# Performance work log

Hardware: AMD Instinct MI355X
Metric: run time of the kernel (lower is better)

The kernel has to match this reference:

```python
import jax, jax.numpy as jnp
import numpy as np

N_NODES = 50000
N_EDGES = 800000
D = 128


def gin_layer(x, edge_index, edge_attr, ee1, ee2, W1, b1, W2, b2):
    # PyG default flow source_to_target: x_j = x[edge_index[0]], aggregate at edge_index[1]
    src, dst = edge_index[0], edge_index[1]
    edge_emb = ee1[edge_attr[:, 0]] + ee2[edge_attr[:, 1]]           # [E, D]
    msg = x[src] + edge_emb                                          # [E, D]
    aggr = jax.ops.segment_sum(msg, dst, num_segments=x.shape[0])    # [N, D]
    h = jax.nn.relu(aggr @ W1 + b1)                                  # [N, 2D]
    return h @ W2 + b2                                               # [N, out]


def setup_inputs() -> dict:
    key = jax.random.key(0)
    ks = jax.random.split(key, 16)
    s = 1.0 / np.sqrt(D)
    inp = {
        "x": jax.random.normal(ks[0], (N_NODES, D), jnp.float32),
        "edge_index": jax.random.randint(ks[1], (2, N_EDGES), 0, N_NODES, dtype=jnp.int32),
        "edge_attr": jax.random.randint(ks[2], (N_EDGES, 2), 0, 3, dtype=jnp.int32),
        "ee1_0": jax.random.normal(ks[3], (6, D), jnp.float32) * s,
        "ee2_0": jax.random.normal(ks[4], (3, D), jnp.float32) * s,
        "W1_0": jax.random.normal(ks[5], (D, 2 * D), jnp.float32) * s,
        "b1_0": jnp.zeros((2 * D,), jnp.float32),
        "W2_0": jax.random.normal(ks[6], (2 * D, D), jnp.float32) * s,
        "b2_0": jnp.zeros((D,), jnp.float32),
        "ee1_1": jax.random.normal(ks[7], (6, D), jnp.float32) * s,
        "ee2_1": jax.random.normal(ks[8], (3, D), jnp.float32) * s,
        "W1_1": jax.random.normal(ks[9], (D, 2 * D), jnp.float32) * s,
        "b1_1": jnp.zeros((2 * D,), jnp.float32),
        "W2_1": jax.random.normal(ks[10], (2 * D, D), jnp.float32) * s,
        "b2_1": jnp.zeros((D,), jnp.float32),
    }
    return inp


def reference(x, edge_index, edge_attr, ee1_0, ee2_0, W1_0, b1_0, W2_0, b2_0,
              ee1_1, ee2_1, W1_1, b1_1, W2_1, b2_1):
    h = gin_layer(x, edge_index, edge_attr, ee1_0, ee2_0, W1_0, b1_0, W2_0, b2_0)
    h = jax.nn.relu(h)  # activation between GNN layers
    out = gin_layer(h, edge_index, edge_attr, ee1_1, ee2_1, W1_1, b1_1, W2_1, b2_1)
    return out  # jk='last'
```

## Files before the change

kernel.cpp:

```cpp
#include <hip/hip_runtime.h>

typedef __attribute__((ext_vector_type(8))) short s16x8;
typedef __attribute__((ext_vector_type(4))) float f32x4;
typedef unsigned short u16;
typedef unsigned char u8;
typedef unsigned long long u64;

#define D_FEAT 128
#define TILE1 4096

__device__ __forceinline__ u16 f2bf(float f) {
    unsigned u = __builtin_bit_cast(unsigned, f);
    u = u + 0x7fffu + ((u >> 16) & 1u);
    return (u16)(u >> 16);
}

__global__ __launch_bounds__(256) void prep_kernel(
        const float4* __restrict__ X4, u16* __restrict__ xb, int n4, int nbA,
        const int* __restrict__ dst, int* __restrict__ ghist, int E, int nb1, int bins,
        const float* __restrict__ ee1_0, const float* __restrict__ ee2_0,
        const float* __restrict__ ee1_1, const float* __restrict__ ee2_1,
        float* __restrict__ emb,
        const float* __restrict__ W1_0, const float* __restrict__ W2_0,
        const float* __restrict__ W1_1, const float* __restrict__ W2_1,
        u16* __restrict__ wout) {
    __shared__ int h[256];
    const int t = threadIdx.x;
    int b = blockIdx.x;

    if (b < nbA) {
        for (int i = b * 256 + t; i < n4; i += nbA * 256) {
            float4 v = X4[i];
            uint2 p;
            p.x = (unsigned)f2bf(v.x) | ((unsigned)f2bf(v.y) << 16);
            p.y = (unsigned)f2bf(v.z) | ((unsigned)f2bf(v.w) << 16);
            *(uint2*)(xb + (size_t)i * 4) = p;
        }
        return;
    }
    b -= nbA;
    if (b < nb1) {
        h[t] = 0;
        __syncthreads();
        const int base = b * TILE1;
        #pragma unroll
        for (int j = 0; j < TILE1 / 256; ++j) {
            int e = base + j * 256 + t;
            if (e < E) atomicAdd(&h[dst[e] >> 8], 1);
        }
        __syncthreads();
        if (t < bins) ghist[t * nb1 + b] = h[t];
        return;
    }
    b -= nb1;
    if (b < 18) {
        int gi = b * 256 + t;
        int layer = gi / 2304;
        int rem = gi - layer * 2304;
        int code = rem >> 7;
        int d = rem & 127;
        int a0 = code / 3, a1 = code - a0 * 3;
        const float* e1 = layer ? ee1_1 : ee1_0;
        const float* e2 = layer ? ee2_1 : ee2_0;
        emb[layer * 2304 + code * 128 + d] = e1[a0 * 128 + d] + e2[a1 * 128 + d];
        return;
    }
    b -= 18;
    {
        int mat = b >> 7;
        const float* s = (mat == 0) ? W1_0 : (mat == 1) ? W2_0 : (mat == 2) ? W1_1 : W2_1;
        int K = (mat & 1) ? 256 : 128;
        int Nc = 384 - K;
        u16* d = wout + mat * 32768;
        int idx = (b & 127) * 256 + t;
        int n = idx / K, k = idx - n * K;
        d[idx] = f2bf(s[k * Nc + n]);
    }
}

__global__ __launch_bounds__(256) void scan1a_kernel(int* __restrict__ ghist,
                                                     int* __restrict__ btot, int nb1) {
    __shared__ int wt[4];
    const int t = threadIdx.x, lane = t & 63, wid = t >> 6;
    const int bin = blockIdx.x;
    const int v = (t < nb1) ? ghist[bin * nb1 + t] : 0;
    int s = v;
    #pragma unroll
    for (int off = 1; off < 64; off <<= 1) {
        int u = __shfl_up(s, off, 64);
        if (lane >= off) s += u;
    }
    if (lane == 63) wt[wid] = s;
    __syncthreads();
    int add = 0;
    #pragma unroll
    for (int w = 0; w < 4; ++w) add += (w < wid) ? wt[w] : 0;
    s += add;
    if (t < nb1) ghist[bin * nb1 + t] = s - v;
    if (t == 255) btot[bin] = s;
}

__global__ __launch_bounds__(256) void scatter1_kernel(const int* __restrict__ src,
                                                       const int* __restrict__ dst,
                                                       const int* __restrict__ eattr,
                                                       const int* __restrict__ ghist,
                                                       const int* __restrict__ btot,
                                                       u64* __restrict__ buf1,
                                                       int E, int nb1, int bins) {
    __shared__ int lofs[256];
    __shared__ int wt[4];
    const int t = threadIdx.x, lane = t & 63, wid = t >> 6;
    const int v = (t < bins) ? btot[t] : 0;
    int s = v;
    #pragma unroll
    for (int off = 1; off < 64; off <<= 1) {
        int u = __shfl_up(s, off, 64);
        if (lane >= off) s += u;
    }
    if (lane == 63) wt[wid] = s;
    __syncthreads();
    int add = 0;
    #pragma unroll
    for (int w = 0; w < 4; ++w) add += (w < wid) ? wt[w] : 0;
    s += add;
    if (t < bins) lofs[t] = (s - v) + ghist[t * nb1 + blockIdx.x];
    __syncthreads();

    const int base = blockIdx.x * TILE1;
    #pragma unroll
    for (int j = 0; j < TILE1 / 256; ++j) {
        int e = base + j * 256 + t;
        if (e < E) {
            int d = dst[e];
            int2 at = ((const int2*)eattr)[e];
            unsigned pay = (unsigned)src[e] | ((unsigned)(at.x * 3 + at.y) << 16);
            int pos = atomicAdd(&lofs[d >> 8], 1);
            buf1[pos] = ((u64)(unsigned)d << 32) | pay;
        }
    }
}

__global__ __launch_bounds__(1024) void bucket2_kernel(const u64* __restrict__ buf1,
                                                       const int* __restrict__ btot,
                                                       int* __restrict__ row_start,
                                                       unsigned* __restrict__ edges,
                                                       unsigned* __restrict__ countsw,
                                                       int N, int bins) {
    __shared__ int cnt[256];
    __shared__ int cur[256];
    __shared__ int wts[4];
    __shared__ unsigned ccnt[256 * 18];
    __shared__ int sb[2];
    const int t = threadIdx.x, lane = t & 63, wid = t >> 6;
    const int bin = blockIdx.x;

    int v0 = 0, s0 = 0;
    if (t < 256) {
        v0 = (t < bins) ? btot[t] : 0;
        s0 = v0;
        #pragma unroll
        for (int off = 1; off < 64; off <<= 1) {
            int u = __shfl_up(s0, off, 64);
            if (lane >= off) s0 += u;
        }
        if (lane == 63) wts[wid] = s0;
        cnt[t] = 0;
    }
    for (int i = t; i < 256 * 18; i += 1024) ccnt[i] = 0;
    __syncthreads();
    if (t < 256) {
        int add = 0;
        #pragma unroll
        for (int w = 0; w < 4; ++w) add += (w < wid) ? wts[w] : 0;
        s0 += add;
        if (t == bin) { sb[0] = s0 - v0; sb[1] = s0; }
    }
    __syncthreads();
    const int lo = sb[0], hi = sb[1];

    for (int i = lo + t; i < hi; i += 1024)
        atomicAdd(&cnt[(int)(buf1[i] >> 32) & 255], 1);
    __syncthreads();

    int v1 = 0, s1 = 0;
    if (t < 256) {
        v1 = cnt[t];
        s1 = v1;
        #pragma unroll
        for (int off = 1; off < 64; off <<= 1) {
            int u = __shfl_up(s1, off, 64);
            if (lane >= off) s1 += u;
        }
        if (lane == 63) wts[wid] = s1;
    }
    __syncthreads();
    if (t < 256) {
        int add = 0;
        #pragma unroll
        for (int w = 0; w < 4; ++w) add += (w < wid) ? wts[w] : 0;
        s1 += add;
        const int g = bin * 256 + t;
        if (g < N) row_start[g + 1] = lo + s1;
        cur[t] = s1 - v1;
        if (bin == 0 && t == 0) row_start[0] = 0;
    }
    __syncthreads();

    for (int i = lo + t; i < hi; i += 1024) {
        u64 rec = buf1[i];
        const int local = (int)(rec >> 32) & 255;
        int loc = atomicAdd(&cur[local], 1);
        edges[lo + loc] = (unsigned)rec;
        atomicAdd(&ccnt[local * 18 + ((unsigned)rec >> 16)], 1);
    }
    __syncthreads();

    if (t < 256) {
        const int g = bin * 256 + t;
        if (g < N) {
            unsigned w[5] = {0, 0, 0, 0, 0};
            #pragma unroll
            for (int c = 0; c < 18; ++c)
                w[c >> 2] |= ccnt[t * 18 + c] << (8 * (c & 3));
            #pragma unroll
            for (int k = 0; k < 5; ++k)
                countsw[(size_t)g * 5 + k] = w[k];
        }
    }
}

__global__ __launch_bounds__(256) void aggregate_kernel(const u16* __restrict__ X,
                                                        const int* __restrict__ row_start,
                                                        const unsigned* __restrict__ edges,
                                                        const float* __restrict__ emb,
                                                        const unsigned* __restrict__ countsw,
                                                        u16* __restrict__ A, int N) {
    __shared__ float semb[18 * 128];
    for (int i = threadIdx.x; i < 18 * 128; i += 256) semb[i] = emb[i];
    __syncthreads();
    const int lane = threadIdx.x & 63;
    const int wstart = blockIdx.x * 4 + (threadIdx.x >> 6);
    const int wstride = gridDim.x * 4;
    const float2* sem2 = (const float2*)semb;

    for (int node = wstart; node < N; node += wstride) {
        unsigned cw[5];
        #pragma unroll
        for (int k = 0; k < 5; ++k) cw[k] = countsw[(size_t)node * 5 + k];

        int s = __builtin_amdgcn_readfirstlane(row_start[node]);
        const int e = __builtin_amdgcn_readfirstlane(row_start[node + 1]);
        float a0 = 0.f, a1 = 0.f;

        while (s < e) {
            const int take = (e - s < 64) ? (e - s) : 64;
            unsigned pl = edges[s + (lane < take ? lane : 0)];
            #pragma unroll
            for (int c = 0; c < 4; ++c) {
                const int cb = c * 16;
                if (cb < take) {
                    unsigned ps[16];
                    unsigned xv[16];
                    #pragma unroll
                    for (int j = 0; j < 16; ++j)
                        ps[j] = __builtin_amdgcn_readlane(pl, cb + j);
                    #pragma unroll
                    for (int j = 0; j < 16; ++j)
                        xv[j] = *(const unsigned*)(X + (ps[j] & 0xFFFFu) * D_FEAT + lane * 2);
                    #pragma unroll
                    for (int j = 0; j < 16; ++j) {
                        const float m = (cb + j < take) ? 1.f : 0.f;
                        a0 += m * __builtin_bit_cast(float, xv[j] << 16);
                        a1 += m * __builtin_bit_cast(float, xv[j] & 0xFFFF0000u);
                    }
                }
            }
            s += take;
        }

        #pragma unroll
        for (int w = 0; w < 5; ++w) {
            #pragma unroll
            for (int b = 0; b < 4; ++b) {
                const int code = w * 4 + b;
                if (code < 18) {
                    const float cf = (float)((cw[w] >> (8 * b)) & 255u);
                    float2 ev = sem2[code * 64 + lane];
                    a0 += cf * ev.x;
                    a1 += cf * ev.y;
                }
            }
        }

        unsigned outp = (unsigned)f2bf(a0) | ((unsigned)f2bf(a1) << 16);
        *(unsigned*)(A + (size_t)node * D_FEAT + lane * 2) = outp;
    }
}

template <bool RELU2, bool OUTF32>
__global__ __launch_bounds__(256, 1) void mlp_kernel(const u16* __restrict__ A,
                                                     const u16* __restrict__ B1t,
                                                     const float* __restrict__ bias1,
                                                     const u16* __restrict__ B2t,
                                                     const float* __restrict__ bias2,
                                                     void* __restrict__ C, int M, int nt) {
    extern __shared__ __align__(16) u16 lds[];
    u16* w1 = lds;
    u16* w2 = lds + 32768;
    u16* hh = lds + 65536;
    const int tid = threadIdx.x;
    const int wave = tid >> 6;
    const int lane = tid & 63;
    const int m16 = lane & 15;
    const int quad = lane >> 4;

    {
        const uint4* src1 = (const uint4*)B1t;
        const uint4* src2 = (const uint4*)B2t;
        #pragma unroll
        for (int i = 0; i < 16; ++i) {
            int s = i * 256 + tid;
            uint4 v = src1[s];
            int c = (((s >> 8) * 4 + ((s >> 2) & 3)) << 6) | ((s & 3) << 4) | ((s >> 4) & 15);
            *(uint4*)(w1 + c * 8) = v;
        }
        #pragma unroll
        for (int i = 0; i < 16; ++i) {
            int s = i * 256 + tid;
            uint4 v = src2[s];
            int c = (((s >> 9) * 8 + ((s >> 2) & 7)) << 6) | ((s & 3) << 4) | ((s >> 5) & 15);
            *(uint4*)(w2 + c * 8) = v;
        }
    }
    float b1v[16];
    #pragma unroll
    for (int t = 0; t < 16; ++t) b1v[t] = bias1[t * 16 + m16];
    float b2v[8];
    #pragma unroll
    for (int t = 0; t < 8; ++t) b2v[t] = bias2[t * 16 + m16];

    const int hbase = wave * 4096;

    int tile = blockIdx.x;
    s16x8 af[4];
    #pragma unroll
    for (int kb = 0; kb < 4; ++kb) af[kb] = s16x8{};
    if (tile < nt) {
        const int arow = tile * 64 + wave * 16 + m16;
        if (arow < M) {
            #pragma unroll
            for (int kb = 0; kb < 4; ++kb)
                af[kb] = *(const s16x8*)(A + (size_t)arow * 128 + kb * 32 + quad * 8);
        }
    }

    __syncthreads();

    for (; tile < nt; tile += 256) {
        const int row0 = tile * 64 + wave * 16;

        f32x4 acc[16];
        #pragma unroll
        for (int t = 0; t < 16; ++t) acc[t] = f32x4{0, 0, 0, 0};
        #pragma unroll
        for (int kb = 0; kb < 4; ++kb) {
            #pragma unroll
            for (int t = 0; t < 16; ++t) {
                s16x8 bf = *(const s16x8*)(w1 + (((((t << 2) | kb) << 6) | lane) * 8));
                acc[t] = __builtin_amdgcn_mfma_f32_16x16x32_bf16(af[kb], bf, acc[t], 0, 0, 0);
            }
        }

        const int ntile = tile + 256;
        s16x8 afn[4];
        #pragma unroll
        for (int kb = 0; kb < 4; ++kb) afn[kb] = s16x8{};
        if (ntile < nt) {
            const int arow = ntile * 64 + wave * 16 + m16;
            if (arow < M) {
                #pragma unroll
                for (int kb = 0; kb < 4; ++kb)
                    afn[kb] = *(const s16x8*)(A + (size_t)arow * 128 + kb * 32 + quad * 8);
            }
        }

        #pragma unroll
        for (int t = 0; t < 16; ++t) {
            const int col = t * 16 + m16;
            #pragma unroll
            for (int r = 0; r < 4; ++r) {
                const int row = quad * 4 + r;
                float v = acc[t][r] + b1v[t];
                v = v > 0.f ? v : 0.f;
                hh[(hbase + row * 256 + col) ^ ((row & 7) << 3)] = f2bf(v);
            }
        }
        __syncthreads();

        f32x4 acc2[8];
        #pragma unroll
        for (int t = 0; t < 8; ++t) acc2[t] = f32x4{0, 0, 0, 0};
        #pragma unroll
        for (int kb = 0; kb < 8; ++kb) {
            s16x8 haf = *(const s16x8*)(hh + ((hbase + m16 * 256 + kb * 32 + quad * 8) ^ ((m16 & 7) << 3)));
            #pragma unroll
            for (int t = 0; t < 8; ++t) {
                s16x8 bf = *(const s16x8*)(w2 + (((((t << 3) | kb) << 6) | lane) * 8));
                acc2[t] = __builtin_amdgcn_mfma_f32_16x16x32_bf16(haf, bf, acc2[t], 0, 0, 0);
            }
        }

        #pragma unroll
        for (int t = 0; t < 8; ++t) {
            const int col = t * 16 + m16;
            #pragma unroll
            for (int r = 0; r < 4; ++r) {
                const int row = row0 + quad * 4 + r;
                if (row < M) {
                    float v = acc2[t][r] + b2v[t];
                    if (RELU2) v = v > 0.f ? v : 0.f;
                    if (OUTF32) ((float*)C)[(size_t)row * 128 + col] = v;
                    else        ((u16*)C)[(size_t)row * 128 + col] = f2bf(v);
                }
            }
        }
        __syncthreads();

        #pragma unroll
        for (int kb = 0; kb < 4; ++kb) af[kb] = afn[kb];
    }
}

extern "C" void kernel_launch(void* const* d_in, const int* in_sizes, int n_in,
                              void* d_out, int out_size, void* d_ws, size_t ws_size,
                              hipStream_t stream) {
    const int N = in_sizes[0] / D_FEAT;
    const int E = in_sizes[1] / 2;

    const float* x    = (const float*)d_in[0];
    const int* eidx   = (const int*)d_in[1];
    const int* eattr  = (const int*)d_in[2];
    const float* ee1_0 = (const float*)d_in[3];
    const float* ee2_0 = (const float*)d_in[4];
    const float* W1_0  = (const float*)d_in[5];
    const float* b1_0  = (const float*)d_in[6];
    const float* W2_0  = (const float*)d_in[7];
    const float* b2_0  = (const float*)d_in[8];
    const float* ee1_1 = (const float*)d_in[9];
    const float* ee2_1 = (const float*)d_in[10];
    const float* W1_1  = (const float*)d_in[11];
    const float* b1_1  = (const float*)d_in[12];
    const float* W2_1  = (const float*)d_in[13];
    const float* b2_1  = (const float*)d_in[14];

    const int nb1  = (E + TILE1 - 1) / TILE1;
    const int bins = (N + 255) / 256;

    char* ws = (char*)d_ws;
    size_t off = 0;
    auto alloc = [&](size_t bytes) { size_t o = off; off = (off + bytes + 255) & ~(size_t)255; return o; };
    size_t o_rowstart = alloc((size_t)(N + 4) * 4);
    size_t o_edges    = alloc((size_t)E * 4);
    size_t o_ghist    = alloc((size_t)bins * nb1 * 4);
    size_t o_btot     = alloc((size_t)bins * 4);
    size_t o_counts   = alloc((size_t)N * 20);
    size_t o_emb      = alloc(2 * 18 * 128 * 4);
    size_t o_wt       = alloc(4 * 32768 * 2);
    size_t o_aa       = alloc((size_t)N * D_FEAT * 2);

    int*      row_start = (int*)(ws + o_rowstart);
    unsigned* edges     = (unsigned*)(ws + o_edges);
    int*      ghist     = (int*)(ws + o_ghist);
    int*      btot      = (int*)(ws + o_btot);
    unsigned* countsw   = (unsigned*)(ws + o_counts);
    float*    emb       = (float*)(ws + o_emb);
    u16*      W1t_0     = (u16*)(ws + o_wt);
    u16*      W2t_0     = W1t_0 + 32768;
    u16*      W1t_1     = W2t_0 + 32768;
    u16*      W2t_1     = W1t_1 + 32768;
    u16*      AA        = (u16*)(ws + o_aa);
    u64*      buf1      = (u64*)(ws + o_aa);

    u16* X2 = (u16*)d_out;
    u16* xb = (u16*)d_out + (size_t)N * D_FEAT;

    const int nt = (N + 63) / 64;
    const int n4 = N * D_FEAT / 4;
    const int nbA = 1024;
    const int aggB = 2048;
    const int LDS_MLP = 163840;

    static bool attr_done = false;
    if (!attr_done) {
        hipFuncSetAttribute((const void*)mlp_kernel<true, false>,
                            hipFuncAttributeMaxDynamicSharedMemorySize, LDS_MLP);
        hipFuncSetAttribute((const void*)mlp_kernel<false, true>,
                            hipFuncAttributeMaxDynamicSharedMemorySize, LDS_MLP);
        attr_done = true;
    }

    prep_kernel<<<nbA + nb1 + 18 + 512, 256, 0, stream>>>(
        (const float4*)x, xb, n4, nbA,
        eidx + E, ghist, E, nb1, bins,
        ee1_0, ee2_0, ee1_1, ee2_1, emb,
        W1_0, W2_0, W1_1, W2_1, W1t_0);

    scan1a_kernel<<<bins, 256, 0, stream>>>(ghist, btot, nb1);
    scatter1_kernel<<<nb1, 256, 0, stream>>>(eidx, eidx + E, eattr, ghist, btot, buf1, E, nb1, bins);
    bucket2_kernel<<<bins, 1024, 0, stream>>>(buf1, btot, row_start, edges, countsw, N, bins);

    aggregate_kernel<<<aggB, 256, 0, stream>>>(xb, row_start, edges, emb, countsw, AA, N);
    mlp_kernel<true, false><<<256, 256, LDS_MLP, stream>>>(AA, W1t_0, b1_0, W2t_0, b2_0, X2, N, nt);

    aggregate_kernel<<<aggB, 256, 0, stream>>>(X2, row_start, edges, emb + 18 * 128, countsw, AA, N);
    mlp_kernel<false, true><<<256, 256, LDS_MLP, stream>>>(AA, W1t_1, b1_1, W2t_1, b2_1, d_out, N, nt);
}
```

Baseline: 264.1 us.

## Hold MLP weight fragments in registers and launch one block per row tile

The weights are pre-swizzled in prep_kernel straight into MFMA fragment order. The MLP kernel no longer stages the full W1/W2 into 160KB of LDS per persistent block. Instead each wave loads its own column slice of the weights into registers, and one block handles a single 64-row tile. This removes the large per-block LDS weight staging and the persistent loop, and allows two blocks per CU. The cost is that every block reloads its weight fragments from global/L2 memory, and register pressure rises with the 4x4 accumulator tiling.

```diff
diff --git a/kernel.cpp b/kernel.cpp
--- a/kernel.cpp
+++ b/kernel.cpp
@@ -69,12 +69,20 @@
     {
         int mat = b >> 7;
         const float* s = (mat == 0) ? W1_0 : (mat == 1) ? W2_0 : (mat == 2) ? W1_1 : W2_1;
-        int K = (mat & 1) ? 256 : 128;
-        int Nc = 384 - K;
         u16* d = wout + mat * 32768;
-        int idx = (b & 127) * 256 + t;
-        int n = idx / K, k = idx - n * K;
-        d[idx] = f2bf(s[k * Nc + n]);
+        int o = (b & 127) * 256 + t;
+        int n, k;
+        if (mat & 1) {
+            const int tt = o >> 12, kb = (o >> 9) & 7, lane = (o >> 3) & 63, j = o & 7;
+            n = tt * 16 + (lane & 15);
+            k = kb * 32 + (lane >> 4) * 8 + j;
+            d[o] = f2bf(s[k * 128 + n]);
+        } else {
+            const int tt = o >> 11, kb = (o >> 9) & 3, lane = (o >> 3) & 63, j = o & 7;
+            n = tt * 16 + (lane & 15);
+            k = kb * 32 + (lane >> 4) * 8 + j;
+            d[o] = f2bf(s[k * 256 + n]);
+        }
     }
 }
 
@@ -298,136 +306,119 @@
 }
 
 template <bool RELU2, bool OUTF32>
-__global__ __launch_bounds__(256, 1) void mlp_kernel(const u16* __restrict__ A,
-                                                     const u16* __restrict__ B1t,
+__global__ __launch_bounds__(256, 2) void mlp_kernel(const u16* __restrict__ A,
+                                                     const u16* __restrict__ F1,
                                                      const float* __restrict__ bias1,
-                                                     const u16* __restrict__ B2t,
+                                                     const u16* __restrict__ F2,
                                                      const float* __restrict__ bias2,
-                                                     void* __restrict__ C, int M, int nt) {
-    extern __shared__ __align__(16) u16 lds[];
-    u16* w1 = lds;
-    u16* w2 = lds + 32768;
-    u16* hh = lds + 65536;
+                                                     void* __restrict__ C, int M) {
+    __shared__ __align__(16) u16 hh[64 * 256];
     const int tid = threadIdx.x;
-    const int wave = tid >> 6;
+    const int w = tid >> 6;
     const int lane = tid & 63;
     const int m16 = lane & 15;
     const int quad = lane >> 4;
-
-    {
-        const uint4* src1 = (const uint4*)B1t;
-        const uint4* src2 = (const uint4*)B2t;
-        #pragma unroll
-        for (int i = 0; i < 16; ++i) {
-            int s = i * 256 + tid;
-            uint4 v = src1[s];
-            int c = (((s >> 8) * 4 + ((s >> 2) & 3)) << 6) | ((s & 3) << 4) | ((s >> 4) & 15);
-            *(uint4*)(w1 + c * 8) = v;
-        }
-        #pragma unroll
-        for (int i = 0; i < 16; ++i) {
-            int s = i * 256 + tid;
-            uint4 v = src2[s];
-            int c = (((s >> 9) * 8 + ((s >> 2) & 7)) << 6) | ((s & 3) << 4) | ((s >> 5) & 15);
-            *(uint4*)(w2 + c * 8) = v;
-        }
-    }
-    float b1v[16];
-    #pragma unroll
-    for (int t = 0; t < 16; ++t) b1v[t] = bias1[t * 16 + m16];
-    float b2v[8];
-    #pragma unroll
-    for (int t = 0; t < 8; ++t) b2v[t] = bias2[t * 16 + m16];
-
-    const int hbase = wave * 4096;
-
-    int tile = blockIdx.x;
-    s16x8 af[4];
-    #pragma unroll
-    for (int kb = 0; kb < 4; ++kb) af[kb] = s16x8{};
-    if (tile < nt) {
-        const int arow = tile * 64 + wave * 16 + m16;
-        if (arow < M) {
-            #pragma unroll
-            for (int kb = 0; kb < 4; ++kb)
-                af[kb] = *(const s16x8*)(A + (size_t)arow * 128 + kb * 32 + quad * 8);
-        }
-    }
-
-    __syncthreads();
-
-    for (; tile < nt; tile += 256) {
-        const int row0 = tile * 64 + wave * 16;
-
-        f32x4 acc[16];
-        #pragma unroll
-        for (int t = 0; t < 16; ++t) acc[t] = f32x4{0, 0, 0, 0};
-        #pragma unroll
-        for (int kb = 0; kb < 4; ++kb) {
-            #pragma unroll
-            for (int t = 0; t < 16; ++t) {
-                s16x8 bf = *(const s16x8*)(w1 + (((((t << 2) | kb) << 6) | lane) * 8));
-                acc[t] = __builtin_amdgcn_mfma_f32_16x16x32_bf16(af[kb], bf, acc[t], 0, 0, 0);
+    const int row0 = blockIdx.x * 64;
+
+    s16x8 af[4][4];
+    #pragma unroll
+    for (int rf = 0; rf < 4; ++rf) {
+        const int arow = row0 + rf * 16 + m16;
+        const bool ok = arow < M;
+        #pragma unroll
+        for (int kb = 0; kb < 4; ++kb)
+            af[rf][kb] = ok ? *(const s16x8*)(A + (size_t)arow * 128 + kb * 32 + quad * 8)
+                            : s16x8{};
+    }
+
+    s16x8 b1f[4][4];
+    #pragma unroll
+    for (int ct = 0; ct < 4; ++ct)
+        #pragma unroll
+        for (int kb = 0; kb < 4; ++kb)
+            b1f[ct][kb] = *(const s16x8*)(F1 + (size_t)(((w * 4 + ct) * 4 + kb) * 64 + lane) * 8);
+
+    float b1v[4];
+    #pragma unroll
+    for (int ct = 0; ct < 4; ++ct) b1v[ct] = bias1[(w * 4 + ct) * 16 + m16];
+
+    f32x4 acc[4][4];
+    #pragma unroll
+    for (int rf = 0; rf < 4; ++rf)
+        #pragma unroll
+        for (int ct = 0; ct < 4; ++ct) acc[rf][ct] = f32x4{0, 0, 0, 0};
+    #pragma unroll
+    for (int kb = 0; kb < 4; ++kb)
+        #pragma unroll
+        for (int rf = 0; rf < 4; ++rf)
+            #pragma unroll
+            for (int ct = 0; ct < 4; ++ct)
+                acc[rf][ct] = __builtin_amdgcn_mfma_f32_16x16x32_bf16(af[rf][kb], b1f[ct][kb],
+                                                                     acc[rf][ct], 0, 0, 0);
+
+    #pragma unroll
+    for (int rf = 0; rf < 4; ++rf) {
+        #pragma unroll
+        for (int ct = 0; ct < 4; ++ct) {
+            const int col = (w * 4 + ct) * 16 + m16;
+            #pragma unroll
+            for (int r = 0; r < 4; ++r) {
+                const int lr = quad * 4 + r;
+                float v = acc[rf][ct][r] + b1v[ct];
+                v = v > 0.f ? v : 0.f;
+                hh[((rf * 16 + lr) * 256 + col) ^ ((lr & 7) << 3)] = f2bf(v);
             }
         }
-
-        const int ntile = tile + 256;
-        s16x8 afn[4];
-        #pragma unroll
-        for (int kb = 0; kb < 4; ++kb) afn[kb] = s16x8{};
-        if (ntile < nt) {
-            const int arow = ntile * 64 + wave * 16 + m16;
-            if (arow < M) {
-                #pragma unroll
-                for (int kb = 0; kb < 4; ++kb)
-                    afn[kb] = *(const s16x8*)(A + (size_t)arow * 128 + kb * 32 + quad * 8);
-            }
-        }
-
-        #pragma unroll
-        for (int t = 0; t < 16; ++t) {
-            const int col = t * 16 + m16;
+    }
+
+    s16x8 b2f[2][8];
+    #pragma unroll
+    for (int ct2 = 0; ct2 < 2; ++ct2)
+        #pragma unroll
+        for (int kb = 0; kb < 8; ++kb)
+            b2f[ct2][kb] = *(const s16x8*)(F2 + (size_t)(((w * 2 + ct2) * 8 + kb) * 64 + lane) * 8);
+    float b2v[2];
+    #pragma unroll
+    for (int ct2 = 0; ct2 < 2; ++ct2) b2v[ct2] = bias2[(w * 2 + ct2) * 16 + m16];
+
+    __syncthreads();
+
+    f32x4 acc2[4][2];
+    #pragma unroll
+    for (int rf = 0; rf < 4; ++rf)
+        #pragma unroll
+        for (int ct2 = 0; ct2 < 2; ++ct2) acc2[rf][ct2] = f32x4{0, 0, 0, 0};
+    #pragma unroll
+    for (int kb = 0; kb < 8; ++kb) {
+        s16x8 haf[4];
+        #pragma unroll
+        for (int rf = 0; rf < 4; ++rf)
+            haf[rf] = *(const s16x8*)(hh + (((rf * 16 + m16) * 256 + kb * 32 + quad * 8)
+                                            ^ ((m16 & 7) << 3)));
+        #pragma unroll
+        for (int rf = 0; rf < 4; ++rf)
+            #pragma unroll
+            for (int ct2 = 0; ct2 < 2; ++ct2)
+                acc2[rf][ct2] = __builtin_amdgcn_mfma_f32_16x16x32_bf16(haf[rf], b2f[ct2][kb],
+                                                                       acc2[rf][ct2], 0, 0, 0);
+    }
+
+    #pragma unroll
+    for (int rf = 0; rf < 4; ++rf) {
+        #pragma unroll
+        for (int ct2 = 0; ct2 < 2; ++ct2) {
+            const int col = (w * 2 + ct2) * 16 + m16;
             #pragma unroll
             for (int r = 0; r < 4; ++r) {
-                const int row = quad * 4 + r;
-                float v = acc[t][r] + b1v[t];
-                v = v > 0.f ? v : 0.f;
-                hh[(hbase + row * 256 + col) ^ ((row & 7) << 3)] = f2bf(v);
-            }
-        }
-        __syncthreads();
-
-        f32x4 acc2[8];
-        #pragma unroll
-        for (int t = 0; t < 8; ++t) acc2[t] = f32x4{0, 0, 0, 0};
-        #pragma unroll
-        for (int kb = 0; kb < 8; ++kb) {
-            s16x8 haf = *(const s16x8*)(hh + ((hbase + m16 * 256 + kb * 32 + quad * 8) ^ ((m16 & 7) << 3)));
-            #pragma unroll
-            for (int t = 0; t < 8; ++t) {
-                s16x8 bf = *(const s16x8*)(w2 + (((((t << 3) | kb) << 6) | lane) * 8));
-                acc2[t] = __builtin_amdgcn_mfma_f32_16x16x32_bf16(haf, bf, acc2[t], 0, 0, 0);
-            }
-        }
-
-        #pragma unroll
-        for (int t = 0; t < 8; ++t) {
-            const int col = t * 16 + m16;
-            #pragma unroll
-            for (int r = 0; r < 4; ++r) {
-                const int row = row0 + quad * 4 + r;
+                const int row = row0 + rf * 16 + quad * 4 + r;
                 if (row < M) {
-                    float v = acc2[t][r] + b2v[t];
+                    float v = acc2[rf][ct2][r] + b2v[ct2];
                     if (RELU2) v = v > 0.f ? v : 0.f;
                     if (OUTF32) ((float*)C)[(size_t)row * 128 + col] = v;
                     else        ((u16*)C)[(size_t)row * 128 + col] = f2bf(v);
                 }
             }
         }
-        __syncthreads();
-
-        #pragma unroll
-        for (int kb = 0; kb < 4; ++kb) af[kb] = afn[kb];
     }
 }
 
@@ -474,10 +465,10 @@
     int*      btot      = (int*)(ws + o_btot);
     unsigned* countsw   = (unsigned*)(ws + o_counts);
     float*    emb       = (float*)(ws + o_emb);
-    u16*      W1t_0     = (u16*)(ws + o_wt);
-    u16*      W2t_0     = W1t_0 + 32768;
-    u16*      W1t_1     = W2t_0 + 32768;
-    u16*      W2t_1     = W1t_1 + 32768;
+    u16*      F1_0      = (u16*)(ws + o_wt);
+    u16*      F2_0      = F1_0 + 32768;
+    u16*      F1_1      = F2_0 + 32768;
+    u16*      F2_1      = F1_1 + 32768;
     u16*      AA        = (u16*)(ws + o_aa);
     u64*      buf1      = (u64*)(ws + o_aa);
 
@@ -488,30 +479,20 @@
     const int n4 = N * D_FEAT / 4;
     const int nbA = 1024;
     const int aggB = 2048;
-    const int LDS_MLP = 163840;
-
-    static bool attr_done = false;
-    if (!attr_done) {
-        hipFuncSetAttribute((const void*)mlp_kernel<true, false>,
-                            hipFuncAttributeMaxDynamicSharedMemorySize, LDS_MLP);
-        hipFuncSetAttribute((const void*)mlp_kernel<false, true>,
-                            hipFuncAttributeMaxDynamicSharedMemorySize, LDS_MLP);
-        attr_done = true;
-    }
 
     prep_kernel<<<nbA + nb1 + 18 + 512, 256, 0, stream>>>(
         (const float4*)x, xb, n4, nbA,
         eidx + E, ghist, E, nb1, bins,
         ee1_0, ee2_0, ee1_1, ee2_1, emb,
-        W1_0, W2_0, W1_1, W2_1, W1t_0);
+        W1_0, W2_0, W1_1, W2_1, F1_0);
 
     scan1a_kernel<<<bins, 256, 0, stream>>>(ghist, btot, nb1);
     scatter1_kernel<<<nb1, 256, 0, stream>>>(eidx, eidx + E, eattr, ghist, btot, buf1, E, nb1, bins);
     bucket2_kernel<<<bins, 1024, 0, stream>>>(buf1, btot, row_start, edges, countsw, N, bins);
 
     aggregate_kernel<<<aggB, 256, 0, stream>>>(xb, row_start, edges, emb, countsw, AA, N);
-    mlp_kernel<true, false><<<256, 256, LDS_MLP, stream>>>(AA, W1t_0, b1_0, W2t_0, b2_0, X2, N, nt);
+    mlp_kernel<true, false><<<nt, 256, 0, stream>>>(AA, F1_0, b1_0, F2_0, b2_0, X2, N);
 
     aggregate_kernel<<<aggB, 256, 0, stream>>>(X2, row_start, edges, emb + 18 * 128, countsw, AA, N);
-    mlp_kernel<false, true><<<256, 256, LDS_MLP, stream>>>(AA, W1t_1, b1_1, W2t_1, b2_1, d_out, N, nt);
-}
+    mlp_kernel<false, true><<<nt, 256, 0, stream>>>(AA, F1_1, b1_1, F2_1, b2_1, d_out, N);
+}
```

Result: faster. 256.9 us, median of 2 (-2.7%).
